# Optimization experiments

Hardware: AMD Instinct MI355X
Metric: run time of the kernel (lower is better)

## Reference

```python
import jax, jax.numpy as jnp
import numpy as np

C_IN = 256
C_INTER = C_IN // 2  # max(1, C//2)
B, D, H, W = 2, 16, 64, 64


def setup_inputs() -> dict:
    key = jax.random.key(0)
    ks = jax.random.split(key, 9)
    s = 1.0 / np.sqrt(C_IN)
    si = 1.0 / np.sqrt(C_INTER)
    return {
        "x": jax.random.normal(ks[0], (B, C_IN, D, H, W), dtype=jnp.float32),
        # 1x1x1 conv weights reduce to [out, in] matrices
        "g_w": jax.random.normal(ks[1], (C_INTER, C_IN), dtype=jnp.float32) * s,
        "g_b": jax.random.normal(ks[2], (C_INTER,), dtype=jnp.float32) * s,
        "theta_w": jax.random.normal(ks[3], (C_INTER, C_IN), dtype=jnp.float32) * s,
        "theta_b": jax.random.normal(ks[4], (C_INTER,), dtype=jnp.float32) * s,
        "phi_w": jax.random.normal(ks[5], (C_INTER, C_IN), dtype=jnp.float32) * s,
        "phi_b": jax.random.normal(ks[6], (C_INTER,), dtype=jnp.float32) * s,
        # note: torch code inits W to zero; random here so gradients/outputs are non-trivial
        "W_w": jax.random.normal(ks[7], (C_IN, C_INTER), dtype=jnp.float32) * si,
        "W_b": jax.random.normal(ks[8], (C_IN,), dtype=jnp.float32) * si,
    }


def reference(x, g_w, g_b, theta_w, theta_b, phi_w, phi_b, W_w, W_b):
    b, c, d, h, w = x.shape
    n = d * h * w
    xf = x.reshape(b, c, n)  # [B, C, N]
    # 1x1x1 convs == per-position linear projections
    g = jnp.einsum('oc,bcn->bon', g_w, xf) + g_b[None, :, None]        # [B, Ci, N]
    th = jnp.einsum('oc,bcn->bon', theta_w, xf) + theta_b[None, :, None]
    ph = jnp.einsum('oc,bcn->bon', phi_w, xf) + phi_b[None, :, None]
    # f = theta^T @ phi (N x N), y = (f / N) @ g^T. Since the normalizer is a
    # constant, reassociate: kv = phi @ g^T is [Ci, Ci], avoiding the NxN matrix.
    kv = jnp.einsum('bin,bjn->bij', ph, g)                              # [B, Ci, Ci]
    y = jnp.einsum('bin,bij->bjn', th, kv) / n                          # [B, Ci, N]
    y = jnp.einsum('oc,bcn->bon', W_w, y) + W_b[None, :, None]          # [B, C, N]
    return x + y.reshape(b, c, d, h, w)
```

## Files before the change

### kernel.cpp

```cpp
#include <hip/hip_runtime.h>

#define NB 2
#define CC 256
#define CI 128
#define NN 65536
#define LDA 72
#define LDX 264

typedef __bf16 bf16x8 __attribute__((ext_vector_type(8)));
typedef float f32x4 __attribute__((ext_vector_type(4)));

__device__ __forceinline__ unsigned short f2bf(float f) {
  unsigned u = __float_as_uint(f);
  u += 0x7fffu + ((u >> 16) & 1u);
  return (unsigned short)(u >> 16);
}

__global__ __launch_bounds__(512) void nl3d_syrk2(const float* __restrict__ x,
                                                  float* __restrict__ S,
                                                  float* __restrict__ partials,
                                                  float* __restrict__ svec,
                                                  int kchunk, int use_partial) {
  __shared__ unsigned short lds[2][256 * LDA];
  const int tid = threadIdx.x;
  const int lane = tid & 63;
  const int wv = tid >> 6;
  const int wm = wv & 3, wn = wv >> 2;
  const int b = blockIdx.y;
  const int kc0 = blockIdx.x * kchunk;

  const float* xb = x + (size_t)b * CC * NN;
  f32x4 acc[4][8];
  const f32x4 zero4 = {0.f, 0.f, 0.f, 0.f};
#pragma unroll
  for (int i = 0; i < 4; ++i)
#pragma unroll
    for (int j = 0; j < 8; ++j) acc[i][j] = zero4;

  float rsum[8];
#pragma unroll
  for (int i = 0; i < 8; ++i) rsum[i] = 0.f;

  const int r0 = tid >> 4;
  const int c4 = tid & 15;
  const int m = lane & 15;
  const int kg = (lane >> 4) * 8;

  const int stages = kchunk >> 6;

  {
    float4 f[8];
#pragma unroll
    for (int i = 0; i < 8; ++i)
      f[i] = *(const float4*)(xb + (size_t)(r0 + 32 * i) * NN + kc0 + c4 * 4);
#pragma unroll
    for (int i = 0; i < 8; ++i) {
      int row = r0 + 32 * i;
      ushort4 h;
      h.x = f2bf(f[i].x); h.y = f2bf(f[i].y); h.z = f2bf(f[i].z); h.w = f2bf(f[i].w);
      *(ushort4*)&lds[0][row * LDA + c4 * 4] = h;
      rsum[i] += f[i].x + f[i].y + f[i].z + f[i].w;
    }
  }
  __syncthreads();

  int cur = 0;
  for (int s = 0; s < stages; ++s) {
    float4 g[8];
    const bool pf = (s + 1 < stages);
    if (pf) {
      const int kc = kc0 + (s + 1) * 64;
#pragma unroll
      for (int i = 0; i < 8; ++i)
        g[i] = *(const float4*)(xb + (size_t)(r0 + 32 * i) * NN + kc + c4 * 4);
    }

    const unsigned short* L = lds[cur];
#pragma unroll
    for (int kk = 0; kk < 2; ++kk) {
      bf16x8 afr[4], bfr[8];
#pragma unroll
      for (int mt = 0; mt < 4; ++mt)
        afr[mt] = *(const bf16x8*)&L[(wm * 64 + mt * 16 + m) * LDA + kk * 32 + kg];
#pragma unroll
      for (int nt = 0; nt < 8; ++nt)
        bfr[nt] = *(const bf16x8*)&L[(wn * 128 + nt * 16 + m) * LDA + kk * 32 + kg];
#pragma unroll
      for (int mt = 0; mt < 4; ++mt)
#pragma unroll
        for (int nt = 0; nt < 8; ++nt)
          acc[mt][nt] = __builtin_amdgcn_mfma_f32_16x16x32_bf16(bfr[nt], afr[mt], acc[mt][nt], 0, 0, 0);
    }

    if (pf) {
      unsigned short* Lw = (unsigned short*)lds[cur ^ 1];
#pragma unroll
      for (int i = 0; i < 8; ++i) {
        int row = r0 + 32 * i;
        ushort4 h;
        h.x = f2bf(g[i].x); h.y = f2bf(g[i].y); h.z = f2bf(g[i].z); h.w = f2bf(g[i].w);
        *(ushort4*)&Lw[row * LDA + c4 * 4] = h;
        rsum[i] += g[i].x + g[i].y + g[i].z + g[i].w;
      }
    }
    __syncthreads();
    cur ^= 1;
  }

  const int col = lane & 15;
  const int rq = (lane >> 4) * 4;
  if (use_partial) {
    float* dst = partials + ((size_t)(b * gridDim.x + blockIdx.x)) * (CC * CC);
#pragma unroll
    for (int mt = 0; mt < 4; ++mt) {
      const int gi = wm * 64 + mt * 16 + col;
#pragma unroll
      for (int nt = 0; nt < 8; ++nt) {
        const int gj = wn * 128 + nt * 16 + rq;
        float4 v;
        v.x = acc[mt][nt][0]; v.y = acc[mt][nt][1];
        v.z = acc[mt][nt][2]; v.w = acc[mt][nt][3];
        *(float4*)&dst[(size_t)gi * CC + gj] = v;
      }
    }
  } else {
    float* Sb = S + (size_t)b * CC * CC;
#pragma unroll
    for (int mt = 0; mt < 4; ++mt)
#pragma unroll
      for (int nt = 0; nt < 8; ++nt)
#pragma unroll
        for (int r = 0; r < 4; ++r) {
          int gi = wm * 64 + mt * 16 + col;
          int gj = wn * 128 + nt * 16 + rq + r;
          atomicAdd(&Sb[(size_t)gi * CC + gj], acc[mt][nt][r]);
        }
  }

  __syncthreads();
  float* ldsRS = (float*)lds[0];
  if (tid < 256) ldsRS[tid] = 0.f;
  __syncthreads();
#pragma unroll
  for (int i = 0; i < 8; ++i) atomicAdd(&ldsRS[r0 + 32 * i], rsum[i]);
  __syncthreads();
  if (tid < 256) atomicAdd(&svec[b * CC + tid], ldsRS[tid]);
}

__global__ __launch_bounds__(256) void nl3d_reduce(const float* __restrict__ partials,
                                                   float* __restrict__ S, int splits) {
  const int e = blockIdx.x * 256 + threadIdx.x;
  const int b = e >> 14;
  const int off = e & 16383;
  const float4* p = (const float4*)partials;
  float4 a0 = {0, 0, 0, 0}, a1 = {0, 0, 0, 0};
  const size_t base = (size_t)b * splits * 16384 + off;
  for (int s = 0; s < splits; s += 2) {
    float4 v0 = p[base + (size_t)s * 16384];
    float4 v1 = p[base + (size_t)(s + 1) * 16384];
    a0.x += v0.x; a0.y += v0.y; a0.z += v0.z; a0.w += v0.w;
    a1.x += v1.x; a1.y += v1.y; a1.z += v1.z; a1.w += v1.w;
  }
  float4 r;
  r.x = a0.x + a1.x; r.y = a0.y + a1.y; r.z = a0.z + a1.z; r.w = a0.w + a1.w;
  ((float4*)S)[e] = r;
}

__global__ void nl3d_b0(const float* __restrict__ g_w, float* __restrict__ gwT) {
  int t = blockIdx.x * 256 + threadIdx.x;
  int j = t >> 8, d = t & 255;
  gwT[d * CI + j] = g_w[t];
}

__global__ void nl3d_b1(const float* __restrict__ phi_w, const float* __restrict__ S,
                        float* __restrict__ P) {
  int b = blockIdx.x >> 7, i = blockIdx.x & 127, d = threadIdx.x;
  const float* Sb = S + (size_t)b * CC * CC;
  const float* ph = phi_w + i * CC;
  float a0 = 0.f, a1 = 0.f, a2 = 0.f, a3 = 0.f;
  for (int c = 0; c < CC; c += 4) {
    a0 += ph[c + 0] * Sb[(c + 0) * CC + d];
    a1 += ph[c + 1] * Sb[(c + 1) * CC + d];
    a2 += ph[c + 2] * Sb[(c + 2) * CC + d];
    a3 += ph[c + 3] * Sb[(c + 3) * CC + d];
  }
  P[((size_t)b * CI + i) * CC + d] = (a0 + a1) + (a2 + a3);
}

__global__ void nl3d_b2(const float* __restrict__ P, const float* __restrict__ gwT,
                        const float* __restrict__ svec, const float* __restrict__ phi_w,
                        const float* __restrict__ phi_b, const float* __restrict__ g_b,
                        float* __restrict__ kv) {
  int b = blockIdx.x >> 7, i = blockIdx.x & 127, j = threadIdx.x;
  const float* Pr = P + ((size_t)b * CI + i) * CC;
  const float* sv = svec + b * CC;
  const float* ph = phi_w + i * CC;
  float u0 = 0.f, u1 = 0.f;
  for (int c = 0; c < CC; c += 2) {
    u0 += ph[c] * sv[c];
    u1 += ph[c + 1] * sv[c + 1];
  }
  float a0 = 0.f, a1 = 0.f, v0 = 0.f, v1 = 0.f;
  for (int d = 0; d < CC; d += 2) {
    float gT0 = gwT[d * CI + j], gT1 = gwT[(d + 1) * CI + j];
    a0 += Pr[d] * gT0; a1 += Pr[d + 1] * gT1;
    v0 += sv[d] * gT0; v1 += sv[d + 1] * gT1;
  }
  kv[((size_t)b * CI + i) * CI + j] =
      (a0 + a1) + (u0 + u1) * g_b[j] + phi_b[i] * ((v0 + v1) + (float)NN * g_b[j]);
}

__global__ void nl3d_b3(const float* __restrict__ kv, const float* __restrict__ theta_w,
                        const float* __restrict__ theta_b, float* __restrict__ T2,
                        float* __restrict__ tb2) {
  int b = blockIdx.x >> 7, j = blockIdx.x & 127, c = threadIdx.x;
  const float* kvb = kv + (size_t)b * CI * CI;
  float a0 = 0.f, a1 = 0.f;
  for (int i = 0; i < CI; i += 2) {
    a0 += kvb[i * CI + j] * theta_w[i * CC + c];
    a1 += kvb[(i + 1) * CI + j] * theta_w[(i + 1) * CC + c];
  }
  T2[((size_t)b * CI + j) * CC + c] = a0 + a1;
  if (c == 0) {
    float t = 0.f;
    for (int i = 0; i < CI; ++i) t += kvb[i * CI + j] * theta_b[i];
    tb2[b * CI + j] = t;
  }
}

__global__ void nl3d_b4(const float* __restrict__ T2, const float* __restrict__ tb2,
                        const float* __restrict__ W_w, const float* __restrict__ W_b,
                        unsigned short* __restrict__ Mbf, float* __restrict__ cvec) {
  int b = blockIdx.x >> 8, o = blockIdx.x & 255, c = threadIdx.x;
  const float inv = 1.0f / (float)NN;
  const float* Wr = W_w + o * CI;
  float a0 = 0.f, a1 = 0.f;
  for (int j = 0; j < CI; j += 2) {
    a0 += Wr[j] * T2[((size_t)b * CI + j) * CC + c];
    a1 += Wr[j + 1] * T2[((size_t)b * CI + j + 1) * CC + c];
  }
  Mbf[((size_t)b * CC + o) * CC + c] = f2bf((a0 + a1) * inv);
  if (c == 0) {
    float t = 0.f;
    for (int j = 0; j < CI; ++j) t += Wr[j] * tb2[b * CI + j];
    cvec[b * CC + o] = t * inv + W_b[o];
  }
}

__global__ __launch_bounds__(256) void nl3d_out(const float* __restrict__ x,
                                                const unsigned short* __restrict__ Mbf,
                                                const float* __restrict__ cvec,
                                                float* __restrict__ out) {
  __shared__ unsigned short xT[64 * LDX];
  const int tid = threadIdx.x;
  const int lane = tid & 63;
  const int wv = tid >> 6;
  const int b = blockIdx.y;
  const int n0 = blockIdx.x * 64;

  const float* xb = x + (size_t)b * CC * NN;
  float* ob = out + (size_t)b * CC * NN;

  {
    const int c4 = tid & 15;
#pragma unroll
    for (int i = 0; i < 8; ++i) {
      int p = i * 16 + (tid >> 4);
      float4 f0 = *(const float4*)(xb + (size_t)(2 * p) * NN + n0 + c4 * 4);
      float4 f1 = *(const float4*)(xb + (size_t)(2 * p + 1) * NN + n0 + c4 * 4);
      float a0[4] = {f0.x, f0.y, f0.z, f0.w};
      float a1[4] = {f1.x, f1.y, f1.z, f1.w};
      int ps = p ^ ((c4 & 7) << 2);
#pragma unroll
      for (int j = 0; j < 4; ++j) {
        unsigned pack = (unsigned)f2bf(a0[j]) | ((unsigned)f2bf(a1[j]) << 16);
        *(unsigned*)&xT[(c4 * 4 + j) * LDX + 2 * ps] = pack;
      }
    }
  }
  __syncthreads();

  f32x4 acc[4][4];
  const f32x4 zero4 = {0.f, 0.f, 0.f, 0.f};
#pragma unroll
  for (int i = 0; i < 4; ++i)
#pragma unroll
    for (int j = 0; j < 4; ++j) acc[i][j] = zero4;

  const int m = lane & 15;
  const int kg = (lane >> 4) * 8;
  const unsigned short* Mb = Mbf + (size_t)b * CC * CC;
#pragma unroll
  for (int kc = 0; kc < 8; ++kc) {
    bf16x8 afr[4], bfr[4];
#pragma unroll
    for (int mt = 0; mt < 4; ++mt)
      afr[mt] = *(const bf16x8*)(Mb + (size_t)(wv * 64 + mt * 16 + m) * CC + kc * 32 + kg);
#pragma unroll
    for (int nt = 0; nt < 4; ++nt) {
      int rr = nt * 16 + m;
      int d0 = (kc * 16 + (kg >> 1)) ^ (((rr >> 2) & 7) << 2);
      bfr[nt] = *(const bf16x8*)&xT[rr * LDX + 2 * d0];
    }
#pragma unroll
    for (int mt = 0; mt < 4; ++mt)
#pragma unroll
      for (int nt = 0; nt < 4; ++nt)
        acc[mt][nt] = __builtin_amdgcn_mfma_f32_16x16x32_bf16(afr[mt], bfr[nt], acc[mt][nt], 0, 0, 0);
  }

  const int col = lane & 15;
  const int rquad = (lane >> 4) * 4;
#pragma unroll
  for (int mt = 0; mt < 4; ++mt)
#pragma unroll
    for (int r = 0; r < 4; ++r) {
      int o = wv * 64 + mt * 16 + rquad + r;
      float cv = cvec[b * CC + o];
      const float* xrow = xb + (size_t)o * NN + n0;
      float* orow = ob + (size_t)o * NN + n0;
#pragma unroll
      for (int nt = 0; nt < 4; ++nt) {
        int n = nt * 16 + col;
        orow[n] = xrow[n] + acc[mt][nt][r] + cv;
      }
    }
}

extern "C" void kernel_launch(void* const* d_in, const int* in_sizes, int n_in,
                              void* d_out, int out_size, void* d_ws, size_t ws_size,
                              hipStream_t stream) {
  const float* x       = (const float*)d_in[0];
  const float* g_w     = (const float*)d_in[1];
  const float* g_b     = (const float*)d_in[2];
  const float* theta_w = (const float*)d_in[3];
  const float* theta_b = (const float*)d_in[4];
  const float* phi_w   = (const float*)d_in[5];
  const float* phi_b   = (const float*)d_in[6];
  const float* W_w     = (const float*)d_in[7];
  const float* W_b     = (const float*)d_in[8];
  float* out = (float*)d_out;

  char* ws = (char*)d_ws;
  float* S    = (float*)(ws);
  float* svec = (float*)(ws + 524288);
  float* P    = (float*)(ws + 526336);
  float* gwT  = (float*)(ws + 788480);
  float* kv   = (float*)(ws + 919552);
  float* T2   = (float*)(ws + 1050624);
  float* tb2  = (float*)(ws + 1312768);
  unsigned short* Mbf = (unsigned short*)(ws + 1313792);
  float* cvec = (float*)(ws + 1575936);
  float* partials = (float*)(ws + 2097152);

  int splits = 0;
  for (int c = 128; c >= 8; c >>= 1) {
    if (2097152 + (size_t)NB * c * CC * CC * 4 <= ws_size) { splits = c; break; }
  }

  if (splits > 0) {
    hipMemsetAsync(svec, 0, 2048, stream);
    nl3d_syrk2<<<dim3(splits, NB), 512, 0, stream>>>(x, S, partials, svec,
                                                     NN / splits, 1);
    nl3d_reduce<<<128, 256, 0, stream>>>(partials, S, splits);
  } else {
    hipMemsetAsync(ws, 0, 526336, stream);
    nl3d_syrk2<<<dim3(64, NB), 512, 0, stream>>>(x, S, (float*)ws, svec,
                                                 NN / 64, 0);
  }
  nl3d_b0<<<128, 256, 0, stream>>>(g_w, gwT);
  nl3d_b1<<<NB * CI, 256, 0, stream>>>(phi_w, S, P);
  nl3d_b2<<<NB * CI, 128, 0, stream>>>(P, gwT, svec, phi_w, phi_b, g_b, kv);
  nl3d_b3<<<NB * CI, 256, 0, stream>>>(kv, theta_w, theta_b, T2, tb2);
  nl3d_b4<<<NB * CC, 256, 0, stream>>>(T2, tb2, W_w, W_b, Mbf, cvec);
  nl3d_out<<<dim3(NN / 64, NB), 256, 0, stream>>>(x, Mbf, cvec, out);
}
```

Baseline: 400.7 us.

## Merge transpose into b1, widen reduction unrolls, prefetch MFMA A fragments

Removes the separate g_w transpose launch by folding it into nl3d_b1, whose 256 blocks of 128 threads cover all 32768 elements. The small GEMV kernels (reduce, b1-b4) get more independent accumulators, and the reduce kernel is relaunched as 256 blocks of 128 threads. In nl3d_out, all x loads are issued before conversion, and the global A-fragment load for the next k-chunk is prefetched during the current MFMAs to hide latency. This costs more registers, which may lower occupancy.

```diff
diff --git a/kernel.cpp b/kernel.cpp
--- a/kernel.cpp
+++ b/kernel.cpp
@@ -147,44 +147,57 @@
   if (tid < 256) atomicAdd(&svec[b * CC + tid], ldsRS[tid]);
 }
 
-__global__ __launch_bounds__(256) void nl3d_reduce(const float* __restrict__ partials,
+__global__ __launch_bounds__(128) void nl3d_reduce(const float* __restrict__ partials,
                                                    float* __restrict__ S, int splits) {
-  const int e = blockIdx.x * 256 + threadIdx.x;
+  const int e = blockIdx.x * 128 + threadIdx.x;
   const int b = e >> 14;
   const int off = e & 16383;
   const float4* p = (const float4*)partials;
-  float4 a0 = {0, 0, 0, 0}, a1 = {0, 0, 0, 0};
+  float4 a0 = {0, 0, 0, 0}, a1 = {0, 0, 0, 0}, a2 = {0, 0, 0, 0}, a3 = {0, 0, 0, 0};
   const size_t base = (size_t)b * splits * 16384 + off;
-  for (int s = 0; s < splits; s += 2) {
+  for (int s = 0; s < splits; s += 4) {
     float4 v0 = p[base + (size_t)s * 16384];
     float4 v1 = p[base + (size_t)(s + 1) * 16384];
+    float4 v2 = p[base + (size_t)(s + 2) * 16384];
+    float4 v3 = p[base + (size_t)(s + 3) * 16384];
     a0.x += v0.x; a0.y += v0.y; a0.z += v0.z; a0.w += v0.w;
     a1.x += v1.x; a1.y += v1.y; a1.z += v1.z; a1.w += v1.w;
+    a2.x += v2.x; a2.y += v2.y; a2.z += v2.z; a2.w += v2.w;
+    a3.x += v3.x; a3.y += v3.y; a3.z += v3.z; a3.w += v3.w;
   }
   float4 r;
-  r.x = a0.x + a1.x; r.y = a0.y + a1.y; r.z = a0.z + a1.z; r.w = a0.w + a1.w;
+  r.x = (a0.x + a1.x) + (a2.x + a3.x);
+  r.y = (a0.y + a1.y) + (a2.y + a3.y);
+  r.z = (a0.z + a1.z) + (a2.z + a3.z);
+  r.w = (a0.w + a1.w) + (a2.w + a3.w);
   ((float4*)S)[e] = r;
 }
 
-__global__ void nl3d_b0(const float* __restrict__ g_w, float* __restrict__ gwT) {
-  int t = blockIdx.x * 256 + threadIdx.x;
-  int j = t >> 8, d = t & 255;
-  gwT[d * CI + j] = g_w[t];
-}
-
 __global__ void nl3d_b1(const float* __restrict__ phi_w, const float* __restrict__ S,
+                        const float* __restrict__ g_w, float* __restrict__ gwT,
                         float* __restrict__ P) {
+  if (threadIdx.x < 128) {
+    int t = blockIdx.x * 128 + threadIdx.x;
+    int j = t >> 8, d2 = t & 255;
+    gwT[d2 * CI + j] = g_w[t];
+  }
   int b = blockIdx.x >> 7, i = blockIdx.x & 127, d = threadIdx.x;
   const float* Sb = S + (size_t)b * CC * CC;
   const float* ph = phi_w + i * CC;
   float a0 = 0.f, a1 = 0.f, a2 = 0.f, a3 = 0.f;
-  for (int c = 0; c < CC; c += 4) {
+  float a4 = 0.f, a5 = 0.f, a6 = 0.f, a7 = 0.f;
+  for (int c = 0; c < CC; c += 8) {
     a0 += ph[c + 0] * Sb[(c + 0) * CC + d];
     a1 += ph[c + 1] * Sb[(c + 1) * CC + d];
     a2 += ph[c + 2] * Sb[(c + 2) * CC + d];
     a3 += ph[c + 3] * Sb[(c + 3) * CC + d];
-  }
-  P[((size_t)b * CI + i) * CC + d] = (a0 + a1) + (a2 + a3);
+    a4 += ph[c + 4] * Sb[(c + 4) * CC + d];
+    a5 += ph[c + 5] * Sb[(c + 5) * CC + d];
+    a6 += ph[c + 6] * Sb[(c + 6) * CC + d];
+    a7 += ph[c + 7] * Sb[(c + 7) * CC + d];
+  }
+  P[((size_t)b * CI + i) * CC + d] =
+      ((a0 + a1) + (a2 + a3)) + ((a4 + a5) + (a6 + a7));
 }
 
 __global__ void nl3d_b2(const float* __restrict__ P, const float* __restrict__ gwT,
@@ -195,19 +208,26 @@
   const float* Pr = P + ((size_t)b * CI + i) * CC;
   const float* sv = svec + b * CC;
   const float* ph = phi_w + i * CC;
-  float u0 = 0.f, u1 = 0.f;
-  for (int c = 0; c < CC; c += 2) {
+  float u0 = 0.f, u1 = 0.f, u2 = 0.f, u3 = 0.f;
+  for (int c = 0; c < CC; c += 4) {
     u0 += ph[c] * sv[c];
     u1 += ph[c + 1] * sv[c + 1];
-  }
-  float a0 = 0.f, a1 = 0.f, v0 = 0.f, v1 = 0.f;
-  for (int d = 0; d < CC; d += 2) {
-    float gT0 = gwT[d * CI + j], gT1 = gwT[(d + 1) * CI + j];
-    a0 += Pr[d] * gT0; a1 += Pr[d + 1] * gT1;
-    v0 += sv[d] * gT0; v1 += sv[d + 1] * gT1;
+    u2 += ph[c + 2] * sv[c + 2];
+    u3 += ph[c + 3] * sv[c + 3];
+  }
+  float a0 = 0.f, a1 = 0.f, a2 = 0.f, a3 = 0.f;
+  float v0 = 0.f, v1 = 0.f, v2 = 0.f, v3 = 0.f;
+  for (int d = 0; d < CC; d += 4) {
+    float gT0 = gwT[d * CI + j],       gT1 = gwT[(d + 1) * CI + j];
+    float gT2 = gwT[(d + 2) * CI + j], gT3 = gwT[(d + 3) * CI + j];
+    a0 += Pr[d] * gT0;     a1 += Pr[d + 1] * gT1;
+    a2 += Pr[d + 2] * gT2; a3 += Pr[d + 3] * gT3;
+    v0 += sv[d] * gT0;     v1 += sv[d + 1] * gT1;
+    v2 += sv[d + 2] * gT2; v3 += sv[d + 3] * gT3;
   }
   kv[((size_t)b * CI + i) * CI + j] =
-      (a0 + a1) + (u0 + u1) * g_b[j] + phi_b[i] * ((v0 + v1) + (float)NN * g_b[j]);
+      ((a0 + a1) + (a2 + a3)) + ((u0 + u1) + (u2 + u3)) * g_b[j] +
+      phi_b[i] * (((v0 + v1) + (v2 + v3)) + (float)NN * g_b[j]);
 }
 
 __global__ void nl3d_b3(const float* __restrict__ kv, const float* __restrict__ theta_w,
@@ -215,12 +235,14 @@
                         float* __restrict__ tb2) {
   int b = blockIdx.x >> 7, j = blockIdx.x & 127, c = threadIdx.x;
   const float* kvb = kv + (size_t)b * CI * CI;
-  float a0 = 0.f, a1 = 0.f;
-  for (int i = 0; i < CI; i += 2) {
+  float a0 = 0.f, a1 = 0.f, a2 = 0.f, a3 = 0.f;
+  for (int i = 0; i < CI; i += 4) {
     a0 += kvb[i * CI + j] * theta_w[i * CC + c];
     a1 += kvb[(i + 1) * CI + j] * theta_w[(i + 1) * CC + c];
-  }
-  T2[((size_t)b * CI + j) * CC + c] = a0 + a1;
+    a2 += kvb[(i + 2) * CI + j] * theta_w[(i + 2) * CC + c];
+    a3 += kvb[(i + 3) * CI + j] * theta_w[(i + 3) * CC + c];
+  }
+  T2[((size_t)b * CI + j) * CC + c] = (a0 + a1) + (a2 + a3);
   if (c == 0) {
     float t = 0.f;
     for (int i = 0; i < CI; ++i) t += kvb[i * CI + j] * theta_b[i];
@@ -234,12 +256,14 @@
   int b = blockIdx.x >> 8, o = blockIdx.x & 255, c = threadIdx.x;
   const float inv = 1.0f / (float)NN;
   const float* Wr = W_w + o * CI;
-  float a0 = 0.f, a1 = 0.f;
-  for (int j = 0; j < CI; j += 2) {
+  float a0 = 0.f, a1 = 0.f, a2 = 0.f, a3 = 0.f;
+  for (int j = 0; j < CI; j += 4) {
     a0 += Wr[j] * T2[((size_t)b * CI + j) * CC + c];
     a1 += Wr[j + 1] * T2[((size_t)b * CI + j + 1) * CC + c];
-  }
-  Mbf[((size_t)b * CC + o) * CC + c] = f2bf((a0 + a1) * inv);
+    a2 += Wr[j + 2] * T2[((size_t)b * CI + j + 2) * CC + c];
+    a3 += Wr[j + 3] * T2[((size_t)b * CI + j + 3) * CC + c];
+  }
+  Mbf[((size_t)b * CC + o) * CC + c] = f2bf(((a0 + a1) + (a2 + a3)) * inv);
   if (c == 0) {
     float t = 0.f;
     for (int j = 0; j < CI; ++j) t += Wr[j] * tb2[b * CI + j];
@@ -263,14 +287,20 @@
 
   {
     const int c4 = tid & 15;
+    const int t4 = tid >> 4;
+    float4 f0[8], f1[8];
 #pragma unroll
     for (int i = 0; i < 8; ++i) {
-      int p = i * 16 + (tid >> 4);
-      float4 f0 = *(const float4*)(xb + (size_t)(2 * p) * NN + n0 + c4 * 4);
-      float4 f1 = *(const float4*)(xb + (size_t)(2 * p + 1) * NN + n0 + c4 * 4);
-      float a0[4] = {f0.x, f0.y, f0.z, f0.w};
-      float a1[4] = {f1.x, f1.y, f1.z, f1.w};
+      int p = i * 16 + t4;
+      f0[i] = *(const float4*)(xb + (size_t)(2 * p) * NN + n0 + c4 * 4);
+      f1[i] = *(const float4*)(xb + (size_t)(2 * p + 1) * NN + n0 + c4 * 4);
+    }
+#pragma unroll
+    for (int i = 0; i < 8; ++i) {
+      int p = i * 16 + t4;
       int ps = p ^ ((c4 & 7) << 2);
+      float a0[4] = {f0[i].x, f0[i].y, f0[i].z, f0[i].w};
+      float a1[4] = {f1[i].x, f1[i].y, f1[i].z, f1[i].w};
 #pragma unroll
       for (int j = 0; j < 4; ++j) {
         unsigned pack = (unsigned)f2bf(a0[j]) | ((unsigned)f2bf(a1[j]) << 16);
@@ -290,12 +320,22 @@
   const int m = lane & 15;
   const int kg = (lane >> 4) * 8;
   const unsigned short* Mb = Mbf + (size_t)b * CC * CC;
+
+  bf16x8 afr[4];
+#pragma unroll
+  for (int mt = 0; mt < 4; ++mt)
+    afr[mt] = *(const bf16x8*)(Mb + (size_t)(wv * 64 + mt * 16 + m) * CC + kg);
 #pragma unroll
   for (int kc = 0; kc < 8; ++kc) {
-    bf16x8 afr[4], bfr[4];
-#pragma unroll
-    for (int mt = 0; mt < 4; ++mt)
-      afr[mt] = *(const bf16x8*)(Mb + (size_t)(wv * 64 + mt * 16 + m) * CC + kc * 32 + kg);
+    bf16x8 cur[4];
+#pragma unroll
+    for (int mt = 0; mt < 4; ++mt) cur[mt] = afr[mt];
+    if (kc < 7) {
+#pragma unroll
+      for (int mt = 0; mt < 4; ++mt)
+        afr[mt] = *(const bf16x8*)(Mb + (size_t)(wv * 64 + mt * 16 + m) * CC + (kc + 1) * 32 + kg);
+    }
+    bf16x8 bfr[4];
 #pragma unroll
     for (int nt = 0; nt < 4; ++nt) {
       int rr = nt * 16 + m;
@@ -306,7 +346,7 @@
     for (int mt = 0; mt < 4; ++mt)
 #pragma unroll
       for (int nt = 0; nt < 4; ++nt)
-        acc[mt][nt] = __builtin_amdgcn_mfma_f32_16x16x32_bf16(afr[mt], bfr[nt], acc[mt][nt], 0, 0, 0);
+        acc[mt][nt] = __builtin_amdgcn_mfma_f32_16x16x32_bf16(cur[mt], bfr[nt], acc[mt][nt], 0, 0, 0);
   }
 
   const int col = lane & 15;
@@ -362,14 +402,13 @@
     hipMemsetAsync(svec, 0, 2048, stream);
     nl3d_syrk2<<<dim3(splits, NB), 512, 0, stream>>>(x, S, partials, svec,
                                                      NN / splits, 1);
-    nl3d_reduce<<<128, 256, 0, stream>>>(partials, S, splits);
+    nl3d_reduce<<<256, 128, 0, stream>>>(partials, S, splits);
   } else {
     hipMemsetAsync(ws, 0, 526336, stream);
     nl3d_syrk2<<<dim3(64, NB), 512, 0, stream>>>(x, S, (float*)ws, svec,
                                                  NN / 64, 0);
   }
-  nl3d_b0<<<128, 256, 0, stream>>>(g_w, gwT);
-  nl3d_b1<<<NB * CI, 256, 0, stream>>>(phi_w, S, P);
+  nl3d_b1<<<NB * CI, 256, 0, stream>>>(phi_w, S, g_w, gwT, P);
   nl3d_b2<<<NB * CI, 128, 0, stream>>>(P, gwT, svec, phi_w, phi_b, g_b, kv);
   nl3d_b3<<<NB * CI, 256, 0, stream>>>(kv, theta_w, theta_b, T2, tb2);
   nl3d_b4<<<NB * CC, 256, 0, stream>>>(T2, tb2, W_w, W_b, Mbf, cvec);
```

New measurement: 392.0 us. 1.02x faster.
